# Kernel optimization log

Hardware: AMD Instinct MI355X
Metric: run time of the kernel (lower is better)

## Reference

```python
import jax, jax.numpy as jnp
import numpy as np

N_HEAD = 8
C = 32
M_DIM = 256
N_SEQ = 256
L_RES = 384
SQ_C = 1.0 / np.sqrt(C)


def setup_inputs() -> dict:
    key = jax.random.key(0)
    ks = jax.random.split(key, 10)
    hc = N_HEAD * C
    s = 0.02
    return {
        "m": jax.random.normal(ks[0], (N_SEQ, L_RES, M_DIM), dtype=jnp.float32),
        "ln_gamma": jnp.ones((M_DIM,), jnp.float32),
        "ln_beta": jnp.zeros((M_DIM,), jnp.float32),
        "Wq": jax.random.normal(ks[1], (M_DIM, hc), jnp.float32) * s,
        "Wk": jax.random.normal(ks[2], (M_DIM, hc), jnp.float32) * s,
        "Wv": jax.random.normal(ks[3], (M_DIM, hc), jnp.float32) * s,
        "Wg": jax.random.normal(ks[4], (M_DIM, hc), jnp.float32) * s,
        "bg": jnp.zeros((hc,), jnp.float32),
        "Wo": jax.random.normal(ks[5], (hc, M_DIM), jnp.float32) * s,
        "bo": jnp.zeros((M_DIM,), jnp.float32),
    }


def layer_norm(x, gamma, beta, eps=1e-5):
    mu = jnp.mean(x, axis=-1, keepdims=True)
    var = jnp.var(x, axis=-1, keepdims=True)
    return (x - mu) * jax.lax.rsqrt(var + eps) * gamma + beta


def reference(m, ln_gamma, ln_beta, Wq, Wk, Wv, Wg, bg, Wo, bo):
    N, L, D = m.shape
    x = layer_norm(m, ln_gamma, ln_beta)
    q = (x @ Wq).reshape(N, L, N_HEAD, C)
    k = (x @ Wk).reshape(N, L, N_HEAD, C)
    v = (x @ Wv).reshape(N, L, N_HEAD, C)
    g = jax.nn.sigmoid(x @ Wg + bg).reshape(N, L, N_HEAD, C)
    # attention over the sequence axis (s,t), independent per column l, head h
    att = jnp.einsum('slhc,tlhc->stlh', q, k) * SQ_C
    att = jax.nn.softmax(att, axis=1)
    o = jnp.einsum('stlh,tlhc->slhc', att, v) * g
    return o.reshape(N, L, N_HEAD * C) @ Wo + bo
```

## Files before the change

kernel.cpp:

```cpp
#include <hip/hip_runtime.h>
#include <cstdint>
#include <cstddef>

#define NSEQ 256
#define LRES 384
#define MDIM 256
#define NHEAD 8
#define CDIM 32
#define NL (NSEQ*LRES)
#define SQC 0.17677669529663687f

#define X_OFF    0u
#define WT_OFF   25165824u
#define QKVG_OFF 25493504u
#define PROJ_SZ  25165824u
#define O_OFF    (QKVG_OFF + 4u*PROJ_SZ)

typedef __attribute__((ext_vector_type(8))) __bf16 bf16x8;
typedef __attribute__((ext_vector_type(4))) float f32x4;

__device__ __forceinline__ unsigned short f2bf(float f) {
  unsigned int u = __float_as_uint(f);
  u = (u + 0x7FFFu + ((u >> 16) & 1u)) >> 16;
  return (unsigned short)u;
}
__device__ __forceinline__ unsigned short f2bf_fast(float f) {
  return (unsigned short)((__float_as_uint(f) + 0x8000u) >> 16);
}
__device__ __forceinline__ float bf2f(unsigned short u){ return __uint_as_float(((unsigned int)u) << 16); }

__device__ __forceinline__ void gld16(const void* g, void* l) {
  __builtin_amdgcn_global_load_lds(
      (const __attribute__((address_space(1))) unsigned int*)g,
      (__attribute__((address_space(3))) unsigned int*)l, 16, 0, 0);
}

__global__ __launch_bounds__(256) void ln_kernel(const float* __restrict__ m,
    const float* __restrict__ gamma, const float* __restrict__ beta,
    unsigned short* __restrict__ x)
{
  int row  = blockIdx.x*4 + (threadIdx.x >> 6);
  int lane = threadIdx.x & 63;
  const float4 v = ((const float4*)(m + (size_t)row*MDIM))[lane];
  float s  = v.x + v.y + v.z + v.w;
  float ss = v.x*v.x + v.y*v.y + v.z*v.z + v.w*v.w;
  #pragma unroll
  for (int off = 32; off > 0; off >>= 1) {
    s  += __shfl_xor(s,  off, 64);
    ss += __shfl_xor(ss, off, 64);
  }
  float mu   = s * (1.f/MDIM);
  float var  = ss * (1.f/MDIM) - mu*mu;
  float rstd = rsqrtf(var + 1e-5f);
  float4 gm = ((const float4*)gamma)[lane];
  float4 bt = ((const float4*)beta)[lane];
  ushort4 pk;
  pk.x = f2bf((v.x - mu)*rstd*gm.x + bt.x);
  pk.y = f2bf((v.y - mu)*rstd*gm.y + bt.y);
  pk.z = f2bf((v.z - mu)*rstd*gm.z + bt.z);
  pk.w = f2bf((v.w - mu)*rstd*gm.w + bt.w);
  ((ushort4*)(x + (size_t)row*MDIM))[lane] = pk;
}

__global__ __launch_bounds__(256) void wtr_kernel(
    const float* __restrict__ W0, const float* __restrict__ W1,
    const float* __restrict__ W2, const float* __restrict__ W3,
    const float* __restrict__ W4, unsigned short* __restrict__ wT)
{
  int p = blockIdx.z;
  const float* W = (p==0)?W0:(p==1)?W1:(p==2)?W2:(p==3)?W3:W4;
  __shared__ float tile[32][33];
  int tx = threadIdx.x & 31, ty0 = threadIdx.x >> 5;
  int bi = blockIdx.x*32, bj = blockIdx.y*32;
  #pragma unroll
  for (int r = 0; r < 4; r++) {
    int ty = ty0 + r*8;
    tile[ty][tx] = W[(bi + ty)*MDIM + bj + tx];
  }
  __syncthreads();
  #pragma unroll
  for (int r = 0; r < 4; r++) {
    int ty = ty0 + r*8;
    wT[p*65536 + (bj + ty)*MDIM + bi + tx] = f2bf(tile[tx][ty]);
  }
}

__global__ __launch_bounds__(256) void proj_kernel(const unsigned short* __restrict__ x,
    const unsigned short* __restrict__ wT, const float* __restrict__ bg,
    unsigned short* __restrict__ qkvg)
{
  __shared__ __align__(16) unsigned short As[128*64];
  __shared__ __align__(16) unsigned short Bs[128*64];
  const int bn = blockIdx.x, bm = blockIdx.y;
  const int tid = threadIdx.x;
  const int lane = tid & 63, wave = tid >> 6;
  const int ln = lane & 15, qd = lane >> 4;
  const int wm = (wave >> 1)*64, wn = (wave & 1)*64;
  const int Rbase = bm*128, Nbase = bn*128;

  const int row0 = tid >> 3;
  const int kc   = (tid & 7) ^ (row0 & 7);
  const unsigned short* aS = x + (size_t)(Rbase + row0)*256 + kc*8;
  const unsigned short* bS = wT + (size_t)(bn >> 1)*65536
                           + (size_t)((bn & 1)*128 + row0)*256 + kc*8;
  unsigned short* ldsA = As + wave*512;
  unsigned short* ldsB = Bs + wave*512;

  f32x4 zero = {0.f,0.f,0.f,0.f};
  f32x4 acc[4][4];
  #pragma unroll
  for (int i=0;i<4;i++)
    #pragma unroll
    for (int j=0;j<4;j++) acc[i][j] = zero;

  const uint4* As4 = (const uint4*)As;
  const uint4* Bs4 = (const uint4*)Bs;

  for (int kk = 0; kk < 4; kk++) {
    #pragma unroll
    for (int e = 0; e < 4; e++) {
      gld16(aS + e*8192, ldsA + e*2048);
      gld16(bS + e*8192, ldsB + e*2048);
    }
    aS += 64; bS += 64;
    __syncthreads();
    #pragma unroll
    for (int kh = 0; kh < 2; kh++) {
      bf16x8 af[4], bfr[4];
      #pragma unroll
      for (int i=0;i<4;i++) {
        int r = wm + i*16 + ln;
        af[i] = __builtin_bit_cast(bf16x8, As4[r*8 + ((kh*4 + qd) ^ (r & 7))]);
      }
      #pragma unroll
      for (int j=0;j<4;j++) {
        int r = wn + j*16 + ln;
        bfr[j] = __builtin_bit_cast(bf16x8, Bs4[r*8 + ((kh*4 + qd) ^ (r & 7))]);
      }
      #pragma unroll
      for (int i=0;i<4;i++)
        #pragma unroll
        for (int j=0;j<4;j++)
          acc[i][j] = __builtin_amdgcn_mfma_f32_16x16x32_bf16(af[i], bfr[j], acc[i][j], 0, 0, 0);
    }
    __syncthreads();
  }

  const int p = Nbase >> 8;
  unsigned short* dstBase = qkvg + (size_t)p*PROJ_SZ;
  #pragma unroll
  for (int i=0;i<4;i++) {
    #pragma unroll
    for (int j=0;j<4;j++) {
      int Jc = Nbase + wn + j*16 + ln;
      int j256 = Jc & 255;
      #pragma unroll
      for (int r=0;r<4;r++) {
        int row = Rbase + wm + i*16 + qd*4 + r;
        float val = acc[i][j][r];
        if (p == 3) val = 1.f/(1.f + __expf(-(val + bg[j256])));
        dstBase[(size_t)row*256 + j256] = f2bf(val);
      }
    }
  }
}

__global__ __launch_bounds__(256) void vtr_kernel(const unsigned short* __restrict__ v,
    unsigned short* __restrict__ vt)
{
  __shared__ unsigned short tile[32][33];
  const int st = blockIdx.x;
  const int lh = blockIdx.y;
  const int l = lh >> 3, h = lh & 7;
  int tx = threadIdx.x & 31, ty0 = threadIdx.x >> 5;
  #pragma unroll
  for (int r=0;r<4;r++) {
    int ty = ty0 + r*8;
    tile[ty][tx] = v[((size_t)(st*32 + ty)*384 + l)*256 + h*32 + tx];
  }
  __syncthreads();
  #pragma unroll
  for (int r=0;r<4;r++) {
    int ty = ty0 + r*8;
    vt[(size_t)lh*8192 + ty*256 + st*32 + tx] = tile[tx][ty];
  }
}

__global__ __launch_bounds__(256, 2) void attn_kernel(
    const unsigned short* __restrict__ qkvg,
    const unsigned short* __restrict__ vt,
    unsigned short* __restrict__ o)
{
  const int l = blockIdx.x, h = blockIdx.y;
  const int tid = threadIdx.x;
  const int wave = tid >> 6, lane = tid & 63;
  const int ln = lane & 15, qd = lane >> 4;
  __shared__ __align__(16) unsigned short Pa[16384];
  const uint4* qg = (const uint4*)qkvg;
  const uint4* kg = qg + (size_t)PROJ_SZ/8;
  const uint4* vg = (const uint4*)vt + (size_t)(l*8 + h)*1024;
  const int hq = h*4;
  const int s0 = wave*64;
  const int sw = ln & 7;

  bf16x8 qf[4];
  #pragma unroll
  for (int nj=0;nj<4;nj++)
    qf[nj] = __builtin_bit_cast(bf16x8, qg[((size_t)(s0 + ln + 16*nj)*384 + l)*32 + hq + qd]);

  f32x4 zero = {0.f,0.f,0.f,0.f};
  f32x4 Oacc[2][4];
  #pragma unroll
  for (int mi=0;mi<2;mi++)
    #pragma unroll
    for (int nj=0;nj<4;nj++) Oacc[mi][nj] = zero;
  float rs[4] = {0.f,0.f,0.f,0.f};

  ushort4* Paw = (ushort4*)Pa;
  const uint4* Pa4 = (const uint4*)Pa;
  const int wbw = wave*1024;
  const int wb4 = wave*512;

  for (int c = 0; c < 4; c++) {
    bf16x8 kf[4];
    uint4 vfr[2][2];
    #pragma unroll
    for (int mi=0;mi<4;mi++)
      kf[mi] = __builtin_bit_cast(bf16x8, kg[((size_t)(c*64 + 16*mi + ln)*384 + l)*32 + hq + qd]);
    #pragma unroll
    for (int mi=0;mi<2;mi++)
      #pragma unroll
      for (int ks=0;ks<2;ks++)
        vfr[mi][ks] = vg[(ln + 16*mi)*32 + c*8 + ks*4 + qd];

    #pragma unroll
    for (int nj=0;nj<4;nj++) {
      f32x4 sv[4];
      #pragma unroll
      for (int mi=0;mi<4;mi++)
        sv[mi] = __builtin_amdgcn_mfma_f32_16x16x32_bf16(kf[mi], qf[nj], zero, 0, 0, 0);
      const int srow = ln + 16*nj;
      #pragma unroll
      for (int mi=0;mi<4;mi++) {
        float p0 = __expf(sv[mi][0]*SQC);
        float p1 = __expf(sv[mi][1]*SQC);
        float p2 = __expf(sv[mi][2]*SQC);
        float p3 = __expf(sv[mi][3]*SQC);
        rs[nj] += (p0+p1)+(p2+p3);
        ushort4 pk;
        pk.x = f2bf_fast(p0); pk.y = f2bf_fast(p1);
        pk.z = f2bf_fast(p2); pk.w = f2bf_fast(p3);
        Paw[wbw + srow*16 + (((2*mi + (qd>>1)) ^ sw) << 1) + (qd & 1)] = pk;
      }
    }
    #pragma unroll
    for (int ks=0;ks<2;ks++) {
      bf16x8 pf[4];
      #pragma unroll
      for (int nj=0;nj<4;nj++)
        pf[nj] = __builtin_bit_cast(bf16x8, Pa4[wb4 + (ln + 16*nj)*8 + ((4*ks + qd) ^ sw)]);
      #pragma unroll
      for (int mi=0;mi<2;mi++)
        #pragma unroll
        for (int nj=0;nj<4;nj++)
          Oacc[mi][nj] = __builtin_amdgcn_mfma_f32_16x16x32_bf16(
              __builtin_bit_cast(bf16x8, vfr[mi][ks]), pf[nj], Oacc[mi][nj], 0, 0, 0);
    }
  }

  #pragma unroll
  for (int nj=0;nj<4;nj++) {
    float r = rs[nj];
    r += __shfl_xor(r, 16, 64);
    r += __shfl_xor(r, 32, 64);
    rs[nj] = 1.f / r;
  }

  const unsigned short* gg = qkvg + 3u*(size_t)PROJ_SZ;
  #pragma unroll
  for (int mi=0;mi<2;mi++) {
    #pragma unroll
    for (int nj=0;nj<4;nj++) {
      const int sg = s0 + ln + 16*nj;
      const int c0 = 16*mi + 4*qd;
      const size_t rowOff = ((size_t)sg*384 + l)*256 + h*32 + c0;
      ushort4 gv = *(const ushort4*)(gg + rowOff);
      float inv = rs[nj];
      ushort4 ov;
      ov.x = f2bf(Oacc[mi][nj][0] * inv * bf2f(gv.x));
      ov.y = f2bf(Oacc[mi][nj][1] * inv * bf2f(gv.y));
      ov.z = f2bf(Oacc[mi][nj][2] * inv * bf2f(gv.z));
      ov.w = f2bf(Oacc[mi][nj][3] * inv * bf2f(gv.w));
      *(ushort4*)(o + rowOff) = ov;
    }
  }
}

__global__ __launch_bounds__(256) void out_kernel(const unsigned short* __restrict__ o,
    const unsigned short* __restrict__ wT, const float* __restrict__ bo,
    float* __restrict__ out)
{
  __shared__ __align__(16) unsigned short As[128*64];
  __shared__ __align__(16) unsigned short Bs[128*64];
  const int bn = blockIdx.x, bm = blockIdx.y;
  const int tid = threadIdx.x;
  const int lane = tid & 63, wave = tid >> 6;
  const int ln = lane & 15, qd = lane >> 4;
  const int wm = (wave >> 1)*64, wn = (wave & 1)*64;
  const int Rbase = bm*128, Nbase = bn*128;

  const int row0 = tid >> 3;
  const int kc   = (tid & 7) ^ (row0 & 7);
  const unsigned short* aS = o  + (size_t)(Rbase + row0)*256 + kc*8;
  const unsigned short* bS = wT + 4u*65536 + (size_t)(Nbase + row0)*256 + kc*8;
  unsigned short* ldsA = As + wave*512;
  unsigned short* ldsB = Bs + wave*512;

  f32x4 zero = {0.f,0.f,0.f,0.f};
  f32x4 acc[4][4];
  #pragma unroll
  for (int i=0;i<4;i++)
    #pragma unroll
    for (int j=0;j<4;j++) acc[i][j] = zero;

  const uint4* As4 = (const uint4*)As;
  const uint4* Bs4 = (const uint4*)Bs;

  for (int kk = 0; kk < 4; kk++) {
    #pragma unroll
    for (int e = 0; e < 4; e++) {
      gld16(aS + e*8192, ldsA + e*2048);
      gld16(bS + e*8192, ldsB + e*2048);
    }
    aS += 64; bS += 64;
    __syncthreads();
    #pragma unroll
    for (int kh = 0; kh < 2; kh++) {
      bf16x8 af[4], bfr[4];
      #pragma unroll
      for (int i=0;i<4;i++) {
        int r = wm + i*16 + ln;
        af[i] = __builtin_bit_cast(bf16x8, As4[r*8 + ((kh*4 + qd) ^ (r & 7))]);
      }
      #pragma unroll
      for (int j=0;j<4;j++) {
        int r = wn + j*16 + ln;
        bfr[j] = __builtin_bit_cast(bf16x8, Bs4[r*8 + ((kh*4 + qd) ^ (r & 7))]);
      }
      #pragma unroll
      for (int i=0;i<4;i++)
        #pragma unroll
        for (int j=0;j<4;j++)
          acc[i][j] = __builtin_amdgcn_mfma_f32_16x16x32_bf16(af[i], bfr[j], acc[i][j], 0, 0, 0);
    }
    __syncthreads();
  }

  #pragma unroll
  for (int i=0;i<4;i++) {
    #pragma unroll
    for (int j=0;j<4;j++) {
      int Jc = Nbase + wn + j*16 + ln;
      float bias = bo[Jc];
      #pragma unroll
      for (int r=0;r<4;r++) {
        int row = Rbase + wm + i*16 + qd*4 + r;
        out[(size_t)row*256 + Jc] = acc[i][j][r] + bias;
      }
    }
  }
}

extern "C" void kernel_launch(void* const* d_in, const int* in_sizes, int n_in,
                              void* d_out, int out_size, void* d_ws, size_t ws_size,
                              hipStream_t stream)
{
  const float* m     = (const float*)d_in[0];
  const float* gamma = (const float*)d_in[1];
  const float* beta  = (const float*)d_in[2];
  const float* Wq    = (const float*)d_in[3];
  const float* Wk    = (const float*)d_in[4];
  const float* Wv    = (const float*)d_in[5];
  const float* Wg    = (const float*)d_in[6];
  const float* bg    = (const float*)d_in[7];
  const float* Wo    = (const float*)d_in[8];
  const float* bo    = (const float*)d_in[9];
  float* out = (float*)d_out;
  unsigned short* ws   = (unsigned short*)d_ws;
  unsigned short* x    = ws + X_OFF;
  unsigned short* wT   = ws + WT_OFF;
  unsigned short* qkvg = ws + QKVG_OFF;
  unsigned short* ob   = ws + O_OFF;
  unsigned short* vnat = qkvg + 2u*(size_t)PROJ_SZ;

  hipLaunchKernelGGL(ln_kernel,   dim3(NL/4),      dim3(256), 0, stream, m, gamma, beta, x);
  hipLaunchKernelGGL(wtr_kernel,  dim3(8, 8, 5),   dim3(256), 0, stream, Wq, Wk, Wv, Wg, Wo, wT);
  hipLaunchKernelGGL(proj_kernel, dim3(8, 768),    dim3(256), 0, stream, x, wT, bg, qkvg);
  hipLaunchKernelGGL(vtr_kernel,  dim3(8, 3072),   dim3(256), 0, stream, vnat, x);
  hipLaunchKernelGGL(attn_kernel, dim3(384, 8),    dim3(256), 0, stream, qkvg, x, ob);
  hipLaunchKernelGGL(out_kernel,  dim3(2, 768),    dim3(256), 0, stream, ob, wT, bo, out);
}
```

Baseline: 494.1 us.

## Keep activation rows in registers and sweep all weight tiles per block in GEMMs

The projection and output GEMMs now give each block 64 rows of activations, held in registers for the full K=256. The block then loops over all output-column tiles, streaming 128x256 weight tiles through a 64KB LDS buffer, and prefetches the next tile while the epilogue runs. The aim is to read each activation row from global memory once, not once per column block, at the cost of more LDS per block and heavier register pressure. The attention grid is also swapped so heads of the same column run in adjacent blocks, which may improve cache locality.

Measured after the change: 441.2 us. 1.12x faster.

```diff
diff --git a/kernel.cpp b/kernel.cpp
--- a/kernel.cpp
+++ b/kernel.cpp
@@ -85,81 +85,91 @@
   }
 }
 
-__global__ __launch_bounds__(256) void proj_kernel(const unsigned short* __restrict__ x,
+__global__ __launch_bounds__(256, 2) void proj_kernel(const unsigned short* __restrict__ x,
     const unsigned short* __restrict__ wT, const float* __restrict__ bg,
     unsigned short* __restrict__ qkvg)
 {
-  __shared__ __align__(16) unsigned short As[128*64];
-  __shared__ __align__(16) unsigned short Bs[128*64];
-  const int bn = blockIdx.x, bm = blockIdx.y;
+  __shared__ __align__(16) unsigned short Bs[128*256];
   const int tid = threadIdx.x;
   const int lane = tid & 63, wave = tid >> 6;
   const int ln = lane & 15, qd = lane >> 4;
-  const int wm = (wave >> 1)*64, wn = (wave & 1)*64;
-  const int Rbase = bm*128, Nbase = bn*128;
-
-  const int row0 = tid >> 3;
-  const int kc   = (tid & 7) ^ (row0 & 7);
-  const unsigned short* aS = x + (size_t)(Rbase + row0)*256 + kc*8;
-  const unsigned short* bS = wT + (size_t)(bn >> 1)*65536
-                           + (size_t)((bn & 1)*128 + row0)*256 + kc*8;
-  unsigned short* ldsA = As + wave*512;
-  unsigned short* ldsB = Bs + wave*512;
-
+  const int wm = (wave & 1)*32, wn = (wave >> 1)*64;
+  const int Rbase = blockIdx.x*64;
+
+  const int sro = lane >> 5;
+  const int sco = lane & 31;
+
+  #pragma unroll
+  for (int e = 0; e < 16; e++) {
+    int r = e*8 + wave*2 + sro;
+    gld16(wT + (size_t)r*256 + ((sco ^ (r & 7))*8), Bs + (e*8 + wave*2)*256);
+  }
+
+  bf16x8 afr[2][8];
+  {
+    const uint4* xg4 = (const uint4*)x;
+    #pragma unroll
+    for (int mi = 0; mi < 2; mi++) {
+      size_t row = (size_t)(Rbase + wm + mi*16 + ln);
+      #pragma unroll
+      for (int kc = 0; kc < 8; kc++)
+        afr[mi][kc] = __builtin_bit_cast(bf16x8, xg4[row*32 + kc*4 + qd]);
+    }
+  }
+
+  const uint4* Bs4 = (const uint4*)Bs;
   f32x4 zero = {0.f,0.f,0.f,0.f};
-  f32x4 acc[4][4];
-  #pragma unroll
-  for (int i=0;i<4;i++)
-    #pragma unroll
-    for (int j=0;j<4;j++) acc[i][j] = zero;
-
-  const uint4* As4 = (const uint4*)As;
-  const uint4* Bs4 = (const uint4*)Bs;
-
-  for (int kk = 0; kk < 4; kk++) {
-    #pragma unroll
-    for (int e = 0; e < 4; e++) {
-      gld16(aS + e*8192, ldsA + e*2048);
-      gld16(bS + e*8192, ldsB + e*2048);
-    }
-    aS += 64; bS += 64;
+
+  for (int bn = 0; bn < 8; bn++) {
+    const int p  = bn >> 1;
+    const int nh = (bn & 1)*128;
+    f32x4 acc[2][4];
+    #pragma unroll
+    for (int i=0;i<2;i++)
+      #pragma unroll
+      for (int j=0;j<4;j++) acc[i][j] = zero;
+
     __syncthreads();
     #pragma unroll
-    for (int kh = 0; kh < 2; kh++) {
-      bf16x8 af[4], bfr[4];
-      #pragma unroll
-      for (int i=0;i<4;i++) {
-        int r = wm + i*16 + ln;
-        af[i] = __builtin_bit_cast(bf16x8, As4[r*8 + ((kh*4 + qd) ^ (r & 7))]);
-      }
-      #pragma unroll
-      for (int j=0;j<4;j++) {
+    for (int kc = 0; kc < 8; kc++) {
+      bf16x8 bfr[4];
+      #pragma unroll
+      for (int j = 0; j < 4; j++) {
         int r = wn + j*16 + ln;
-        bfr[j] = __builtin_bit_cast(bf16x8, Bs4[r*8 + ((kh*4 + qd) ^ (r & 7))]);
-      }
-      #pragma unroll
-      for (int i=0;i<4;i++)
+        bfr[j] = __builtin_bit_cast(bf16x8, Bs4[r*32 + ((kc*4 + qd) ^ (r & 7))]);
+      }
+      #pragma unroll
+      for (int mi=0;mi<2;mi++)
         #pragma unroll
         for (int j=0;j<4;j++)
-          acc[i][j] = __builtin_amdgcn_mfma_f32_16x16x32_bf16(af[i], bfr[j], acc[i][j], 0, 0, 0);
+          acc[mi][j] = __builtin_amdgcn_mfma_f32_16x16x32_bf16(afr[mi][kc], bfr[j], acc[mi][j], 0, 0, 0);
     }
     __syncthreads();
-  }
-
-  const int p = Nbase >> 8;
-  unsigned short* dstBase = qkvg + (size_t)p*PROJ_SZ;
-  #pragma unroll
-  for (int i=0;i<4;i++) {
-    #pragma unroll
-    for (int j=0;j<4;j++) {
-      int Jc = Nbase + wn + j*16 + ln;
-      int j256 = Jc & 255;
-      #pragma unroll
-      for (int r=0;r<4;r++) {
-        int row = Rbase + wm + i*16 + qd*4 + r;
-        float val = acc[i][j][r];
-        if (p == 3) val = 1.f/(1.f + __expf(-(val + bg[j256])));
-        dstBase[(size_t)row*256 + j256] = f2bf(val);
+
+    if (bn < 7) {
+      int pn = (bn+1) >> 1, nhn = ((bn+1) & 1)*128;
+      const unsigned short* wbase = wT + (size_t)pn*65536 + (size_t)nhn*256;
+      #pragma unroll
+      for (int e = 0; e < 16; e++) {
+        int r = e*8 + wave*2 + sro;
+        gld16(wbase + (size_t)r*256 + ((sco ^ (r & 7))*8), Bs + (e*8 + wave*2)*256);
+      }
+    }
+
+    unsigned short* dstBase = qkvg + (size_t)p*PROJ_SZ;
+    #pragma unroll
+    for (int mi=0;mi<2;mi++) {
+      #pragma unroll
+      for (int j=0;j<4;j++) {
+        int j256 = nh + wn + j*16 + ln;
+        float bgv = (p == 3) ? bg[j256] : 0.f;
+        #pragma unroll
+        for (int r=0;r<4;r++) {
+          int row = Rbase + wm + mi*16 + qd*4 + r;
+          float val = acc[mi][j][r];
+          if (p == 3) val = 1.f/(1.f + __expf(-(val + bgv)));
+          dstBase[(size_t)row*256 + j256] = f2bf(val);
+        }
       }
     }
   }
@@ -191,7 +201,7 @@
     const unsigned short* __restrict__ vt,
     unsigned short* __restrict__ o)
 {
-  const int l = blockIdx.x, h = blockIdx.y;
+  const int h = blockIdx.x, l = blockIdx.y;
   const int tid = threadIdx.x;
   const int wave = tid >> 6, lane = tid & 63;
   const int ln = lane & 15, qd = lane >> 4;
@@ -296,76 +306,87 @@
   }
 }
 
-__global__ __launch_bounds__(256) void out_kernel(const unsigned short* __restrict__ o,
+__global__ __launch_bounds__(256, 2) void out_kernel(const unsigned short* __restrict__ o,
     const unsigned short* __restrict__ wT, const float* __restrict__ bo,
     float* __restrict__ out)
 {
-  __shared__ __align__(16) unsigned short As[128*64];
-  __shared__ __align__(16) unsigned short Bs[128*64];
-  const int bn = blockIdx.x, bm = blockIdx.y;
+  __shared__ __align__(16) unsigned short Bs[128*256];
   const int tid = threadIdx.x;
   const int lane = tid & 63, wave = tid >> 6;
   const int ln = lane & 15, qd = lane >> 4;
-  const int wm = (wave >> 1)*64, wn = (wave & 1)*64;
-  const int Rbase = bm*128, Nbase = bn*128;
-
-  const int row0 = tid >> 3;
-  const int kc   = (tid & 7) ^ (row0 & 7);
-  const unsigned short* aS = o  + (size_t)(Rbase + row0)*256 + kc*8;
-  const unsigned short* bS = wT + 4u*65536 + (size_t)(Nbase + row0)*256 + kc*8;
-  unsigned short* ldsA = As + wave*512;
-  unsigned short* ldsB = Bs + wave*512;
-
+  const int wm = (wave & 1)*32, wn = (wave >> 1)*64;
+  const int Rbase = blockIdx.x*64;
+  const unsigned short* wo = wT + 4u*65536;
+
+  const int sro = lane >> 5;
+  const int sco = lane & 31;
+
+  #pragma unroll
+  for (int e = 0; e < 16; e++) {
+    int r = e*8 + wave*2 + sro;
+    gld16(wo + (size_t)r*256 + ((sco ^ (r & 7))*8), Bs + (e*8 + wave*2)*256);
+  }
+
+  bf16x8 afr[2][8];
+  {
+    const uint4* og4 = (const uint4*)o;
+    #pragma unroll
+    for (int mi = 0; mi < 2; mi++) {
+      size_t row = (size_t)(Rbase + wm + mi*16 + ln);
+      #pragma unroll
+      for (int kc = 0; kc < 8; kc++)
+        afr[mi][kc] = __builtin_bit_cast(bf16x8, og4[row*32 + kc*4 + qd]);
+    }
+  }
+
+  const uint4* Bs4 = (const uint4*)Bs;
   f32x4 zero = {0.f,0.f,0.f,0.f};
-  f32x4 acc[4][4];
-  #pragma unroll
-  for (int i=0;i<4;i++)
-    #pragma unroll
-    for (int j=0;j<4;j++) acc[i][j] = zero;
-
-  const uint4* As4 = (const uint4*)As;
-  const uint4* Bs4 = (const uint4*)Bs;
-
-  for (int kk = 0; kk < 4; kk++) {
-    #pragma unroll
-    for (int e = 0; e < 4; e++) {
-      gld16(aS + e*8192, ldsA + e*2048);
-      gld16(bS + e*8192, ldsB + e*2048);
-    }
-    aS += 64; bS += 64;
+
+  for (int bn = 0; bn < 2; bn++) {
+    const int nh = bn*128;
+    f32x4 acc[2][4];
+    #pragma unroll
+    for (int i=0;i<2;i++)
+      #pragma unroll
+      for (int j=0;j<4;j++) acc[i][j] = zero;
+
     __syncthreads();
     #pragma unroll
-    for (int kh = 0; kh < 2; kh++) {
-      bf16x8 af[4], bfr[4];
-      #pragma unroll
-      for (int i=0;i<4;i++) {
-        int r = wm + i*16 + ln;
-        af[i] = __builtin_bit_cast(bf16x8, As4[r*8 + ((kh*4 + qd) ^ (r & 7))]);
-      }
-      #pragma unroll
-      for (int j=0;j<4;j++) {
+    for (int kc = 0; kc < 8; kc++) {
+      bf16x8 bfr[4];
+      #pragma unroll
+      for (int j = 0; j < 4; j++) {
         int r = wn + j*16 + ln;
-        bfr[j] = __builtin_bit_cast(bf16x8, Bs4[r*8 + ((kh*4 + qd) ^ (r & 7))]);
-      }
-      #pragma unroll
-      for (int i=0;i<4;i++)
+        bfr[j] = __builtin_bit_cast(bf16x8, Bs4[r*32 + ((kc*4 + qd) ^ (r & 7))]);
+      }
+      #pragma unroll
+      for (int mi=0;mi<2;mi++)
         #pragma unroll
         for (int j=0;j<4;j++)
-          acc[i][j] = __builtin_amdgcn_mfma_f32_16x16x32_bf16(af[i], bfr[j], acc[i][j], 0, 0, 0);
+          acc[mi][j] = __builtin_amdgcn_mfma_f32_16x16x32_bf16(afr[mi][kc], bfr[j], acc[mi][j], 0, 0, 0);
     }
     __syncthreads();
-  }
-
-  #pragma unroll
-  for (int i=0;i<4;i++) {
-    #pragma unroll
-    for (int j=0;j<4;j++) {
-      int Jc = Nbase + wn + j*16 + ln;
-      float bias = bo[Jc];
-      #pragma unroll
-      for (int r=0;r<4;r++) {
-        int row = Rbase + wm + i*16 + qd*4 + r;
-        out[(size_t)row*256 + Jc] = acc[i][j][r] + bias;
+
+    if (bn < 1) {
+      const unsigned short* wbase = wo + 128u*256;
+      #pragma unroll
+      for (int e = 0; e < 16; e++) {
+        int r = e*8 + wave*2 + sro;
+        gld16(wbase + (size_t)r*256 + ((sco ^ (r & 7))*8), Bs + (e*8 + wave*2)*256);
+      }
+    }
+
+    #pragma unroll
+    for (int mi=0;mi<2;mi++) {
+      #pragma unroll
+      for (int j=0;j<4;j++) {
+        int col = nh + wn + j*16 + ln;
+        float bias = bo[col];
+        #pragma unroll
+        for (int r=0;r<4;r++) {
+          int row = Rbase + wm + mi*16 + qd*4 + r;
+          out[(size_t)row*256 + col] = acc[mi][j][r] + bias;
+        }
       }
     }
   }
@@ -395,8 +416,8 @@
 
   hipLaunchKernelGGL(ln_kernel,   dim3(NL/4),      dim3(256), 0, stream, m, gamma, beta, x);
   hipLaunchKernelGGL(wtr_kernel,  dim3(8, 8, 5),   dim3(256), 0, stream, Wq, Wk, Wv, Wg, Wo, wT);
-  hipLaunchKernelGGL(proj_kernel, dim3(8, 768),    dim3(256), 0, stream, x, wT, bg, qkvg);
+  hipLaunchKernelGGL(proj_kernel, dim3(1536),      dim3(256), 0, stream, x, wT, bg, qkvg);
   hipLaunchKernelGGL(vtr_kernel,  dim3(8, 3072),   dim3(256), 0, stream, vnat, x);
-  hipLaunchKernelGGL(attn_kernel, dim3(384, 8),    dim3(256), 0, stream, qkvg, x, ob);
-  hipLaunchKernelGGL(out_kernel,  dim3(2, 768),    dim3(256), 0, stream, ob, wT, bo, out);
-}
+  hipLaunchKernelGGL(attn_kernel, dim3(8, 384),    dim3(256), 0, stream, qkvg, x, ob);
+  hipLaunchKernelGGL(out_kernel,  dim3(1536),      dim3(256), 0, stream, ob, wT, bo, out);
+}
```
